# Performance work log

Measured on AMD Instinct MI355X. Metric: run time of the kernel, lower is better.

The kernel has to match this reference:

```python
import jax, jax.numpy as jnp
import numpy as np

WINDOW_SIZES = [4, 8, 12]
BN_EPS = 1e-5


def conv1x1(x, w, b):
    # x: [B,C,H,W], w: [O,C], b: [O]
    return jnp.einsum('bchw,oc->bohw', x, w) + b[None, :, None, None]


def bnorm(x, gamma, beta, mean, var):
    inv = gamma * jax.lax.rsqrt(var + BN_EPS)
    return (x - mean[None, :, None, None]) * inv[None, :, None, None] + beta[None, :, None, None]


def shift5(x):
    # ShiftConv2d1 depthwise fixed-weight conv == 4-direction zero-padded shift + identity
    b, c, H, W = x.shape
    g = c // 5
    p = jnp.pad(x, ((0, 0), (0, 0), (1, 1), (1, 1)))
    return jnp.concatenate([
        p[:, 0 * g:1 * g, 1:-1, 2:],    # kernel[1,2]: x[i, j+1]
        p[:, 1 * g:2 * g, 1:-1, :-2],   # kernel[1,0]: x[i, j-1]
        p[:, 2 * g:3 * g, 2:, 1:-1],    # kernel[2,1]: x[i+1, j]
        p[:, 3 * g:4 * g, :-2, 1:-1],   # kernel[0,1]: x[i-1, j]
        p[:, 4 * g:, 1:-1, 1:-1],       # kernel[1,1]: identity
    ], axis=1)


def lfe(x, w0, b0, w1, b1):
    y = jax.nn.relu(conv1x1(shift5(x), w0, b0))
    return conv1x1(shift5(y), w1, b1)


def win_part(x, ws):
    # [B,C,H,W] -> [B*nh*nw, ws*ws, C]
    b, c, H, W = x.shape
    x = x.reshape(b, c, H // ws, ws, W // ws, ws)
    return x.transpose(0, 2, 4, 3, 5, 1).reshape(b * (H // ws) * (W // ws), ws * ws, c)


def win_merge(y, ws, b, H, W):
    # [B*nh*nw, ws*ws, C] -> [B,C,H,W]
    c = y.shape[-1]
    y = y.reshape(b, H // ws, W // ws, ws, ws, c)
    return y.transpose(0, 5, 1, 3, 2, 4).reshape(b, c, H, W)


def gmsa_first(x, pi_w, pi_b, bn_g, bn_b, bn_m, bn_v, po_w, po_b):
    b, c, H, W = x.shape
    xp = bnorm(conv1x1(x, pi_w, pi_b), bn_g, bn_b, bn_m, bn_v)
    ch = 2 * c // 3
    ys, atns = [], []
    for i, ws in enumerate(WINDOW_SIZES):
        x_ = xp[:, i * ch:(i + 1) * ch]
        x_ = jnp.roll(x_, (-(ws // 2), -(ws // 2)), axis=(2, 3))
        qv = win_part(x_, ws)                      # [nw, ws*ws, 2*cc]
        cc = ch // 2
        q, v = qv[..., :cc], qv[..., cc:]
        atn = jax.nn.softmax(q @ q.transpose(0, 2, 1), axis=-1)
        y_ = win_merge(atn @ v, ws, b, H, W)
        y_ = jnp.roll(y_, (ws // 2, ws // 2), axis=(2, 3))
        ys.append(y_)
        atns.append(atn)
    return conv1x1(jnp.concatenate(ys, axis=1), po_w, po_b), atns


def gmsa_shared(x, atns, pi_w, pi_b, bn_g, bn_b, bn_m, bn_v, po_w, po_b):
    b, c, H, W = x.shape
    xp = bnorm(conv1x1(x, pi_w, pi_b), bn_g, bn_b, bn_m, bn_v)
    ch = c // 3
    ys = []
    for i, ws in enumerate(WINDOW_SIZES):
        x_ = jnp.roll(xp[:, i * ch:(i + 1) * ch], (-(ws // 2), -(ws // 2)), axis=(2, 3))
        v = win_part(x_, ws)
        y_ = win_merge(atns[i] @ v, ws, b, H, W)
        ys.append(jnp.roll(y_, (ws // 2, ws // 2), axis=(2, 3)))
    return conv1x1(jnp.concatenate(ys, axis=1), po_w, po_b)


def setup_inputs() -> dict:
    key = jax.random.key(0)
    ks = jax.random.split(key, 20)
    B, C, H, W = 4, 60, 384, 384
    E = 2 * C  # exp_ratio=2 hidden width
    s = 0.05

    def rn(k, shape):
        return jax.random.normal(k, shape, dtype=jnp.float32) * s

    return {
        'x': jax.random.normal(ks[0], (B, C, H, W), dtype=jnp.float32),
        # LFE 0
        'lfe0_w0': rn(ks[1], (E, C)), 'lfe0_b0': jnp.zeros((E,), jnp.float32),
        'lfe0_w1': rn(ks[2], (C, E)), 'lfe0_b1': jnp.zeros((C,), jnp.float32),
        # GMSA 0 (calc_attn=True): project_inp C->2C, BN(2C), project_out C->C
        'g0_pi_w': rn(ks[3], (2 * C, C)), 'g0_pi_b': jnp.zeros((2 * C,), jnp.float32),
        'g0_bn_g': jnp.ones((2 * C,), jnp.float32), 'g0_bn_b': jnp.zeros((2 * C,), jnp.float32),
        'g0_bn_m': jnp.zeros((2 * C,), jnp.float32), 'g0_bn_v': jnp.ones((2 * C,), jnp.float32),
        'g0_po_w': rn(ks[4], (C, C)), 'g0_po_b': jnp.zeros((C,), jnp.float32),
        # LFE 1
        'lfe1_w0': rn(ks[5], (E, C)), 'lfe1_b0': jnp.zeros((E,), jnp.float32),
        'lfe1_w1': rn(ks[6], (C, E)), 'lfe1_b1': jnp.zeros((C,), jnp.float32),
        # GMSA 1 (calc_attn=False): project_inp C->C, BN(C), project_out C->C
        'g1_pi_w': rn(ks[7], (C, C)), 'g1_pi_b': jnp.zeros((C,), jnp.float32),
        'g1_bn_g': jnp.ones((C,), jnp.float32), 'g1_bn_b': jnp.zeros((C,), jnp.float32),
        'g1_bn_m': jnp.zeros((C,), jnp.float32), 'g1_bn_v': jnp.ones((C,), jnp.float32),
        'g1_po_w': rn(ks[8], (C, C)), 'g1_po_b': jnp.zeros((C,), jnp.float32),
    }


def reference(x, lfe0_w0, lfe0_b0, lfe0_w1, lfe0_b1,
              g0_pi_w, g0_pi_b, g0_bn_g, g0_bn_b, g0_bn_m, g0_bn_v, g0_po_w, g0_po_b,
              lfe1_w0, lfe1_b0, lfe1_w1, lfe1_b1,
              g1_pi_w, g1_pi_b, g1_bn_g, g1_bn_b, g1_bn_m, g1_bn_v, g1_po_w, g1_po_b):
    # depth 0
    x = lfe(x, lfe0_w0, lfe0_b0, lfe0_w1, lfe0_b1) + x
    y, atns = gmsa_first(x, g0_pi_w, g0_pi_b, g0_bn_g, g0_bn_b, g0_bn_m, g0_bn_v, g0_po_w, g0_po_b)
    x = y + x
    # shared depth 1 (reuses attention maps)
    x = lfe(x, lfe1_w0, lfe1_b0, lfe1_w1, lfe1_b1) + x
    y = gmsa_shared(x, atns, g1_pi_w, g1_pi_b, g1_bn_g, g1_bn_b, g1_bn_m, g1_bn_v, g1_po_w, g1_po_b)
    return y + x
```

## Files before the change

kernel.cpp:

```cpp
#include <hip/hip_runtime.h>
#include <math.h>

constexpr int B_ = 4, C_ = 60, H_ = 384, W_ = 384;
constexpr int HW_ = H_ * W_;
constexpr int NC_ = B_ * C_ * HW_;
constexpr int NE_ = B_ * 120 * HW_;

typedef __attribute__((ext_vector_type(8))) short short8;
typedef __attribute__((ext_vector_type(4))) float f32x4;
typedef __attribute__((ext_vector_type(4))) unsigned short u16x4;

__device__ __forceinline__ unsigned short f2b(float f) {
    unsigned u = __builtin_bit_cast(unsigned, f);
    unsigned r = (u + 0x7fff + ((u >> 16) & 1)) >> 16;
    return (unsigned short)r;
}
__device__ __forceinline__ float b2f(unsigned short s) {
    return __builtin_bit_cast(float, (unsigned)s << 16);
}

__device__ __forceinline__ int xcd_swz(int bid, int nwg) {
    const int q = nwg >> 3, r = nwg & 7;
    const int xcd = bid & 7, off = bid >> 3;
    return (xcd < r ? xcd * (q + 1) : r * (q + 1) + (xcd - r) * q) + off;
}

struct PrepJobs {
    const float* src[8];
    unsigned short* dst[8];
    int cin[8];
    int cout[8];
};

__global__ __launch_bounds__(256) void prep_all(PrepJobs J)
{
    int bid = blockIdx.x;
    #pragma unroll 1
    for (int j = 0; j < 8; ++j) {
        const int KP = J.cin[j]  > 64 ? 128 : 64;
        const int MP = J.cout[j] > 64 ? 128 : 64;
        const int nb = MP * KP / 256;
        if (bid < nb) {
            const int i = bid * 256 + threadIdx.x;
            const int o = i / KP, c = i - o * KP;
            const float v = (o < J.cout[j] && c < J.cin[j]) ? J.src[j][o * J.cin[j] + c] : 0.f;
            J.dst[j][o * KP + (c ^ ((o & 7) << 3))] = f2b(v);
            return;
        }
        bid -= nb;
    }
}

struct ABJobs {
    const float* bias[8];
    const float* g[8];
    const float* bb[8];
    const float* m[8];
    const float* v[8];
    float* dst[8];
    int cout[8];
};

__global__ __launch_bounds__(256) void prep_ab(ABJobs J)
{
    const int j = blockIdx.x;
    const int n = J.cout[j];
    for (int o = threadIdx.x; o < n; o += 256) {
        float A = 1.f, Bv = J.bias[j][o];
        if (J.g[j]) {
            const float s = J.g[j][o] * rsqrtf(J.v[j][o] + 1e-5f);
            A  = s;
            Bv = (Bv - J.m[j][o]) * s + J.bb[j][o];
        }
        J.dst[j][o]     = A;
        J.dst[j][n + o] = Bv;
    }
}

template<int KP>
__device__ __forceinline__ int lds_off(int px, int cb) {
    return px * (KP * 2) + (cb ^ ((px & 7) << 4) ^ (((px >> 3) & 1) << 6));
}

template<int CIN, int COUT, int GSH, bool SRCB, bool RELU, bool RESID,
         bool RESIDB, bool OUTB>
__global__ __launch_bounds__(256, 4)
void conv_g(const void* __restrict__ in_, const unsigned short* __restrict__ wp,
            const float* __restrict__ AB,
            const void* __restrict__ resid_, void* __restrict__ out_)
{
    constexpr int KP  = CIN  > 64 ? 128 : 64;
    constexpr int MP  = COUT > 64 ? 128 : 64;
    constexpr int NNT = MP / 16;
    constexpr int KBL = KP / 32;
    __shared__ __align__(16) char xlds[128 * KP * 2];

    const int tid = threadIdx.x;
    const int n0  = blockIdx.x * 128;
    const int b   = n0 / HW_;
    const int p0  = n0 - b * HW_;
    const int hh  = p0 / W_;
    const int ww0 = p0 - hh * W_;

    for (int task = tid; task < (KP / 2) * 16; task += 256) {
        const int oct = (task >> 4) & 15;
        const int pr  = (task & 15) | ((task >> 8) << 4);
        const int c0  = pr * 2;
        const int s0  = oct * 8;

        if (c0 >= CIN) {
            #pragma unroll
            for (int i = 0; i < 8; ++i)
                *(unsigned*)(xlds + lds_off<KP>(s0 + i, c0 * 2)) = 0u;
            continue;
        }

        int dh = 0, dw = 0;
        if (GSH > 0) {
            const int grp = c0 / GSH;
            dh = (grp == 2) ? 1 : ((grp == 3) ? -1 : 0);
            dw = (grp == 0) ? 1 : ((grp == 1) ? -1 : 0);
        }
        const int h2 = hh + dh;
        const bool vh = (unsigned)h2 < (unsigned)H_;
        const long eoff = (long)(b * CIN + c0) * HW_ + h2 * W_ + ww0 + s0;

        unsigned short va[8], vb[8];
        if (vh) {
            if constexpr (SRCB) {
                const unsigned short* p = (const unsigned short*)in_;
                short8 A = *(const short8*)(p + eoff);
                short8 Bv = *(const short8*)(p + eoff + HW_);
                #pragma unroll
                for (int i = 0; i < 8; ++i) { va[i] = (unsigned short)A[i]; vb[i] = (unsigned short)Bv[i]; }
            } else {
                const float* p = (const float*)in_;
                f32x4 A0 = *(const f32x4*)(p + eoff);
                f32x4 A1 = *(const f32x4*)(p + eoff + 4);
                f32x4 B0 = *(const f32x4*)(p + eoff + HW_);
                f32x4 B1 = *(const f32x4*)(p + eoff + HW_ + 4);
                #pragma unroll
                for (int i = 0; i < 4; ++i) {
                    va[i] = f2b(A0[i]); va[i + 4] = f2b(A1[i]);
                    vb[i] = f2b(B0[i]); vb[i + 4] = f2b(B1[i]);
                }
            }
        } else {
            #pragma unroll
            for (int i = 0; i < 8; ++i) { va[i] = 0; vb[i] = 0; }
        }
        #pragma unroll
        for (int i = 0; i < 8; ++i) {
            const int px = s0 + i - dw;
            if ((unsigned)px < 128u) {
                const unsigned v = (unsigned)va[i] | ((unsigned)vb[i] << 16);
                *(unsigned*)(xlds + lds_off<KP>(px, c0 * 2)) = v;
            }
        }
        if (GSH > 0 && dw != 0) {
            const bool hndl = (dw == 1) ? (oct == 15) : (oct == 0);
            if (hndl) {
                const int px_e = (dw == 1) ? 127 : 0;
                const int w_abs = ww0 + px_e + dw;
                unsigned short ua = 0, ub = 0;
                if (vh && (unsigned)w_abs < (unsigned)W_) {
                    const long e2 = (long)(b * CIN + c0) * HW_ + h2 * W_ + w_abs;
                    if constexpr (SRCB) {
                        ua = ((const unsigned short*)in_)[e2];
                        ub = ((const unsigned short*)in_)[e2 + HW_];
                    } else {
                        ua = f2b(((const float*)in_)[e2]);
                        ub = f2b(((const float*)in_)[e2 + HW_]);
                    }
                }
                *(unsigned*)(xlds + lds_off<KP>(px_e, c0 * 2)) =
                    (unsigned)ua | ((unsigned)ub << 16);
            }
        }
    }
    __syncthreads();

    const int wv = tid >> 6, lo = tid & 15, hi = (tid & 63) >> 4;
    f32x4 acc[2][NNT];
    #pragma unroll
    for (int mt = 0; mt < 2; ++mt)
        #pragma unroll
        for (int nt = 0; nt < NNT; ++nt) acc[mt][nt] = f32x4{0.f, 0.f, 0.f, 0.f};

    #pragma unroll
    for (int kb = 0; kb < KBL; ++kb) {
        short8 a[2], bb[NNT];
        #pragma unroll
        for (int mt = 0; mt < 2; ++mt) {
            const int row = wv * 32 + mt * 16 + lo;
            a[mt] = *(const short8*)(xlds + lds_off<KP>(row, kb * 64 + hi * 16));
        }
        #pragma unroll
        for (int nt = 0; nt < NNT; ++nt) {
            const int row = nt * 16 + lo;
            bb[nt] = *(const short8*)((const char*)wp +
                      row * (KP * 2) + ((kb * 64 + hi * 16) ^ ((row & 7) << 4)));
        }
        #pragma unroll
        for (int mt = 0; mt < 2; ++mt)
            #pragma unroll
            for (int nt = 0; nt < NNT; ++nt)
                acc[mt][nt] = __builtin_amdgcn_mfma_f32_16x16x32_bf16(
                    a[mt], bb[nt], acc[mt][nt], 0, 0, 0);
    }

    #pragma unroll
    for (int mt = 0; mt < 2; ++mt) {
        const int px0 = p0 + wv * 32 + mt * 16 + hi * 4;
        #pragma unroll
        for (int nt = 0; nt < NNT; ++nt) {
            const int ch = nt * 16 + lo;
            if (ch < COUT) {
                const long oi = (long)(b * COUT + ch) * HW_ + px0;
                float v[4];
                f32x4 rf;
                u16x4 rb;
                if (RESID) {
                    if (RESIDB) rb = *(const u16x4*)((const unsigned short*)resid_ + oi);
                    else        rf = *(const f32x4*)((const float*)resid_ + oi);
                }
                #pragma unroll
                for (int r = 0; r < 4; ++r) {
                    float t = fmaf(acc[mt][nt][r], AB[ch], AB[COUT + ch]);
                    if (RELU) t = fmaxf(t, 0.f);
                    if (RESID) t += RESIDB ? b2f(rb[r]) : rf[r];
                    v[r] = t;
                }
                if (OUTB) {
                    u16x4 o4;
                    #pragma unroll
                    for (int r = 0; r < 4; ++r) o4[r] = f2b(v[r]);
                    *(u16x4*)((unsigned short*)out_ + oi) = o4;
                } else {
                    *(f32x4*)((float*)out_ + oi) = f32x4{v[0], v[1], v[2], v[3]};
                }
            }
        }
    }
}

template<int WS, int WPB>
__global__ __launch_bounds__(256)
void attn_m(const unsigned short* __restrict__ qsrc, int qC, int qbase,
            const unsigned short* __restrict__ vsrc, int vC, int vbase,
            unsigned short* __restrict__ out, int obase)
{
    constexpr int P     = WS * WS;
    constexpr int NMT   = P / 16;
    constexpr int S     = WS / 2;
    constexpr int WGX   = W_ / WS;
    constexpr int WGY   = H_ / WS;
    constexpr int NWIN  = WGY * WGX;
    constexpr int QP    = 40;
    constexpr int KP2   = ((P + 31) / 32) * 32;
    constexpr int VP    = KP2 + 8;
    constexpr int KB2   = KP2 / 32;
    constexpr int TILES = WPB * NMT;

    __shared__ __align__(16) unsigned short Qs[WPB * P * QP];
    __shared__ __align__(16) unsigned short VTs[WPB * 32 * VP];
    __shared__ __align__(16) unsigned short Ps[WPB * P * VP];
    __shared__ float rs[WPB * P];

    const int tid = threadIdx.x;
    const int blk = xcd_swz(blockIdx.x, gridDim.x);

    for (int i = tid; i < WPB * P * 6; i += 256) {
        const int row = i / 6, j = i - (i / 6) * 6;
        *(unsigned*)&Qs[row * QP + 20 + 2 * j] = 0u;
    }
    for (int i = tid; i < WPB * 12 * (KP2 / 2); i += 256) {
        const int rr = i / (KP2 / 2), j = i - rr * (KP2 / 2);
        const int win = rr / 12, ch = 20 + (rr - (rr / 12) * 12);
        *(unsigned*)&VTs[(win * 32 + ch) * VP + 2 * j] = 0u;
    }
    if constexpr (KP2 > P) {
        for (int i = tid; i < WPB * 20 * ((KP2 - P) / 2); i += 256) {
            const int rr = i / ((KP2 - P) / 2), j = i - rr * ((KP2 - P) / 2);
            const int win = rr / 20, ch = rr - (rr / 20) * 20;
            *(unsigned*)&VTs[(win * 32 + ch) * VP + P + 2 * j] = 0u;
        }
        for (int i = tid; i < WPB * P * ((KP2 - P) / 2); i += 256) {
            const int row = i / ((KP2 - P) / 2), j = i - row * ((KP2 - P) / 2);
            *(unsigned*)&Ps[row * VP + P + 2 * j] = 0u;
        }
    }
    for (int e = tid; e < WPB * P * 20; e += 256) {
        const int win = e / (P * 20);
        const int rem = e - win * (P * 20);
        const int ch  = rem / P;
        const int pos = rem - ch * P;
        const int gw  = blk * WPB + win;
        const int b   = gw / NWIN;
        const int rwin = gw - b * NWIN;
        const int wh = rwin / WGX, ww = rwin - (rwin / WGX) * WGX;
        const int pr = pos / WS,  pc = pos - (pos / WS) * WS;
        int hs = wh * WS + pr + S; if (hs >= H_) hs -= H_;
        int wd = ww * WS + pc + S; if (wd >= W_) wd -= W_;
        const long off = (long)hs * W_ + wd;
        Qs [(win * P  + pos) * QP + ch ] = qsrc[(long)(b * qC + qbase + ch) * HW_ + off];
        VTs[(win * 32 + ch ) * VP + pos] = vsrc[(long)(b * vC + vbase + ch) * HW_ + off];
    }
    __syncthreads();

    const int wv = tid >> 6, lo = tid & 15, hi = (tid & 63) >> 4;

    for (int t = wv; t < TILES; t += 4) {
        const int win = t / NMT, mt = t - (t / NMT) * NMT;
        const unsigned short* Qw = Qs + win * P * QP;
        unsigned short* Pw = Ps + win * P * VP;

        const short8 af = *(const short8*)(Qw + (mt * 16 + lo) * QP + hi * 8);
        f32x4 a1[NMT];
        #pragma unroll
        for (int nt = 0; nt < NMT; ++nt) a1[nt] = f32x4{0.f, 0.f, 0.f, 0.f};
        #pragma unroll
        for (int nt = 0; nt < NMT; ++nt) {
            const short8 bf = *(const short8*)(Qw + (nt * 16 + lo) * QP + hi * 8);
            a1[nt] = __builtin_amdgcn_mfma_f32_16x16x32_bf16(af, bf, a1[nt], 0, 0, 0);
        }
        float psum[4] = {0.f, 0.f, 0.f, 0.f};
        #pragma unroll
        for (int nt = 0; nt < NMT; ++nt) {
            #pragma unroll
            for (int r = 0; r < 4; ++r) {
                const float p = __expf(a1[nt][r]);
                psum[r] += p;
                Pw[(mt * 16 + hi * 4 + r) * VP + nt * 16 + lo] = f2b(p);
            }
        }
        #pragma unroll
        for (int r = 0; r < 4; ++r) {
            psum[r] += __shfl_xor(psum[r], 1);
            psum[r] += __shfl_xor(psum[r], 2);
            psum[r] += __shfl_xor(psum[r], 4);
            psum[r] += __shfl_xor(psum[r], 8);
        }
        if (lo == 0) {
            #pragma unroll
            for (int r = 0; r < 4; ++r)
                rs[win * P + mt * 16 + hi * 4 + r] = psum[r];
        }
    }
    __syncthreads();

    for (int t = wv; t < TILES; t += 4) {
        const int win = t / NMT, qt = t - (t / NMT) * NMT;
        const unsigned short* Vw = VTs + win * 32 * VP;
        const unsigned short* Pw = Ps + win * P * VP;

        f32x4 a2[2];
        a2[0] = f32x4{0.f, 0.f, 0.f, 0.f};
        a2[1] = f32x4{0.f, 0.f, 0.f, 0.f};
        #pragma unroll
        for (int kb = 0; kb < KB2; ++kb) {
            const short8 bf = *(const short8*)(Pw + (qt * 16 + lo) * VP + kb * 32 + hi * 8);
            #pragma unroll
            for (int m2 = 0; m2 < 2; ++m2) {
                const short8 af = *(const short8*)(Vw + (m2 * 16 + lo) * VP + kb * 32 + hi * 8);
                a2[m2] = __builtin_amdgcn_mfma_f32_16x16x32_bf16(af, bf, a2[m2], 0, 0, 0);
            }
        }
        const int gw = blk * WPB + win;
        const int b  = gw / NWIN;
        const int rwin = gw - b * NWIN;
        const int wh = rwin / WGX, ww = rwin - (rwin / WGX) * WGX;

        const int row = qt * 16 + lo;
        const float inv = 1.f / rs[win * P + row];
        const int pr = row / WS, pc = row - (row / WS) * WS;
        int hs = wh * WS + pr + S; if (hs >= H_) hs -= H_;
        int wd = ww * WS + pc + S; if (wd >= W_) wd -= W_;
        const long pbase = (long)(b * 60 + obase) * HW_ + (long)hs * W_ + wd;
        #pragma unroll
        for (int m2 = 0; m2 < 2; ++m2) {
            #pragma unroll
            for (int r = 0; r < 4; ++r) {
                const int ch = m2 * 16 + hi * 4 + r;
                if (ch < 20)
                    out[pbase + (long)ch * HW_] = f2b(a2[m2][r] * inv);
            }
        }
    }
}

extern "C" void kernel_launch(void* const* d_in, const int* in_sizes, int n_in,
                              void* d_out, int out_size, void* d_ws, size_t ws_size,
                              hipStream_t stream)
{
    const float* x     = (const float*)d_in[0];
    const float* l0w0  = (const float*)d_in[1];
    const float* l0b0  = (const float*)d_in[2];
    const float* l0w1  = (const float*)d_in[3];
    const float* l0b1  = (const float*)d_in[4];
    const float* g0piw = (const float*)d_in[5];
    const float* g0pib = (const float*)d_in[6];
    const float* g0bng = (const float*)d_in[7];
    const float* g0bnb = (const float*)d_in[8];
    const float* g0bnm = (const float*)d_in[9];
    const float* g0bnv = (const float*)d_in[10];
    const float* g0pow = (const float*)d_in[11];
    const float* g0pob = (const float*)d_in[12];
    const float* l1w0  = (const float*)d_in[13];
    const float* l1b0  = (const float*)d_in[14];
    const float* l1w1  = (const float*)d_in[15];
    const float* l1b1  = (const float*)d_in[16];
    const float* g1piw = (const float*)d_in[17];
    const float* g1pib = (const float*)d_in[18];
    const float* g1bng = (const float*)d_in[19];
    const float* g1bnb = (const float*)d_in[20];
    const float* g1bnm = (const float*)d_in[21];
    const float* g1bnv = (const float*)d_in[22];
    const float* g1pow = (const float*)d_in[23];
    const float* g1pob = (const float*)d_in[24];

    unsigned short* HID = (unsigned short*)d_ws;
    unsigned short* XPB = HID + NE_;
    unsigned short* XP1 = XPB + NE_;
    unsigned short* YS1 = XP1 + NC_;
    unsigned short* CCB = YS1 + NC_;
    unsigned short* WP  = CCB + NC_;
    float*          ABF = (float*)(WP + 53248);
    float* OUTF  = (float*)d_out;
    unsigned short* YS0 = (unsigned short*)d_out;

    unsigned short* W1  = WP;
    unsigned short* W2  = WP + 8192;
    unsigned short* W3  = WP + 16384;
    unsigned short* W5  = WP + 24576;
    unsigned short* W6  = WP + 28672;
    unsigned short* W7  = WP + 36864;
    unsigned short* W8  = WP + 45056;
    unsigned short* W10 = WP + 49152;

    float* AB1  = ABF;
    float* AB2  = ABF + 240;
    float* AB3  = ABF + 360;
    float* AB5  = ABF + 600;
    float* AB6  = ABF + 720;
    float* AB7  = ABF + 960;
    float* AB8  = ABF + 1080;
    float* AB10 = ABF + 1200;

    PrepJobs J;
    J.src[0]=l0w0;  J.dst[0]=W1;  J.cin[0]=60;  J.cout[0]=120;
    J.src[1]=l0w1;  J.dst[1]=W2;  J.cin[1]=120; J.cout[1]=60;
    J.src[2]=g0piw; J.dst[2]=W3;  J.cin[2]=60;  J.cout[2]=120;
    J.src[3]=g0pow; J.dst[3]=W5;  J.cin[3]=60;  J.cout[3]=60;
    J.src[4]=l1w0;  J.dst[4]=W6;  J.cin[4]=60;  J.cout[4]=120;
    J.src[5]=l1w1;  J.dst[5]=W7;  J.cin[5]=120; J.cout[5]=60;
    J.src[6]=g1piw; J.dst[6]=W8;  J.cin[6]=60;  J.cout[6]=60;
    J.src[7]=g1pow; J.dst[7]=W10; J.cin[7]=60;  J.cout[7]=60;
    prep_all<<<208, 256, 0, stream>>>(J);

    ABJobs A;
    for (int j = 0; j < 8; ++j) { A.g[j]=nullptr; A.bb[j]=nullptr; A.m[j]=nullptr; A.v[j]=nullptr; }
    A.bias[0]=l0b0;  A.dst[0]=AB1;  A.cout[0]=120;
    A.bias[1]=l0b1;  A.dst[1]=AB2;  A.cout[1]=60;
    A.bias[2]=g0pib; A.dst[2]=AB3;  A.cout[2]=120; A.g[2]=g0bng; A.bb[2]=g0bnb; A.m[2]=g0bnm; A.v[2]=g0bnv;
    A.bias[3]=g0pob; A.dst[3]=AB5;  A.cout[3]=60;
    A.bias[4]=l1b0;  A.dst[4]=AB6;  A.cout[4]=120;
    A.bias[5]=l1b1;  A.dst[5]=AB7;  A.cout[5]=60;
    A.bias[6]=g1pib; A.dst[6]=AB8;  A.cout[6]=60;  A.g[6]=g1bng; A.bb[6]=g1bnb; A.m[6]=g1bnm; A.v[6]=g1bnv;
    A.bias[7]=g1pob; A.dst[7]=AB10; A.cout[7]=60;
    prep_ab<<<8, 256, 0, stream>>>(A);

    dim3 blk(256);
    dim3 gconv(B_ * HW_ / 128);

    conv_g<60,120,12,false,true,false,false,true><<<gconv,blk,0,stream>>>(
        x, W1, AB1, nullptr, HID);
    conv_g<120,60,24,true,false,true,false,true><<<gconv,blk,0,stream>>>(
        HID, W2, AB2, x, CCB);
    conv_g<60,120,0,true,false,false,false,true><<<gconv,blk,0,stream>>>(
        CCB, W3, AB3, nullptr, XPB);
    attn_m<4,4><<<dim3(9216),blk,0,stream>>>(XPB,120,0,   XPB,120,20,  YS0, 0);
    attn_m<8,1><<<dim3(9216),blk,0,stream>>>(XPB,120,40,  XPB,120,60,  YS0,20);
    attn_m<12,1><<<dim3(4096),blk,0,stream>>>(XPB,120,80, XPB,120,100, YS0,40);
    conv_g<60,60,0,true,false,true,true,true><<<gconv,blk,0,stream>>>(
        YS0, W5, AB5, CCB, CCB);
    conv_g<60,120,12,true,true,false,false,true><<<gconv,blk,0,stream>>>(
        CCB, W6, AB6, nullptr, HID);
    conv_g<120,60,24,true,false,true,true,true><<<gconv,blk,0,stream>>>(
        HID, W7, AB7, CCB, CCB);
    conv_g<60,60,0,true,false,false,false,true><<<gconv,blk,0,stream>>>(
        CCB, W8, AB8, nullptr, XP1);
    attn_m<4,4><<<dim3(9216),blk,0,stream>>>(XPB,120,0,  XP1,60,0,  YS1, 0);
    attn_m<8,1><<<dim3(9216),blk,0,stream>>>(XPB,120,40, XP1,60,20, YS1,20);
    attn_m<12,1><<<dim3(4096),blk,0,stream>>>(XPB,120,80,XP1,60,40, YS1,40);
    conv_g<60,60,0,true,false,true,true,false><<<gconv,blk,0,stream>>>(
        YS1, W10, AB10, CCB, OUTF);
}
```

Before: 981.9 us.

## Add specialized 120->60 shift-conv kernel with split-K double-buffered LDS staging

New measurement: 989.0 us. No clear change (+0.7%).

```diff
diff --git a/kernel.cpp b/kernel.cpp
--- a/kernel.cpp
+++ b/kernel.cpp
@@ -239,6 +239,179 @@
                 } else {
                     *(f32x4*)((float*)out_ + oi) = f32x4{v[0], v[1], v[2], v[3]};
                 }
+            }
+        }
+    }
+}
+
+template<bool RESIDB, bool OUTB>
+__global__ __launch_bounds__(256, 4)
+void conv_g2(const unsigned short* __restrict__ in_,
+             const unsigned short* __restrict__ wp,
+             const float* __restrict__ AB,
+             const void* __restrict__ resid_, void* __restrict__ out_)
+{
+    constexpr int COUT = 60;
+    constexpr int NNT  = 4;
+    __shared__ __align__(16) char xlds[2][128 * 128];
+
+    const int tid = threadIdx.x;
+    const int n0  = blockIdx.x * 128;
+    const int b   = n0 / HW_;
+    const int p0  = n0 - b * HW_;
+    const int hh  = p0 / W_;
+    const int ww0 = p0 - hh * W_;
+
+    auto h_load = [&](int task, int h, short8& A, short8& Bv, unsigned& edge) {
+        const int oct = (task >> 5) & 15;
+        const int pr  = task & 31;
+        const int c0g = h * 64 + pr * 2;
+        A = short8{0,0,0,0,0,0,0,0}; Bv = A; edge = 0;
+        if (c0g >= 120) return;
+        const int grp = c0g / 24;
+        const int dh = (grp == 2) ? 1 : ((grp == 3) ? -1 : 0);
+        const int dw = (grp == 0) ? 1 : ((grp == 1) ? -1 : 0);
+        const int h2 = hh + dh;
+        const bool vh = (unsigned)h2 < (unsigned)H_;
+        const int s0 = oct * 8;
+        const long eoff = (long)(b * 120 + c0g) * HW_ + h2 * W_ + ww0 + s0;
+        if (vh) {
+            A  = *(const short8*)(in_ + eoff);
+            Bv = *(const short8*)(in_ + eoff + HW_);
+        }
+        if (dw != 0) {
+            const bool hndl = (dw == 1) ? (oct == 15) : (oct == 0);
+            if (hndl) {
+                const int px_e = (dw == 1) ? 127 : 0;
+                const int w_abs = ww0 + px_e + dw;
+                if (vh && (unsigned)w_abs < (unsigned)W_) {
+                    const long e2 = (long)(b * 120 + c0g) * HW_ + h2 * W_ + w_abs;
+                    edge = (unsigned)in_[e2] | ((unsigned)in_[e2 + HW_] << 16);
+                }
+            }
+        }
+    };
+    auto h_write = [&](int task, int h, short8 A, short8 Bv, unsigned edge) {
+        const int oct = (task >> 5) & 15;
+        const int pr  = task & 31;
+        const int c0g = h * 64 + pr * 2;
+        const int cb  = pr * 4;
+        const int s0  = oct * 8;
+        int dw = 0;
+        if (c0g < 120) {
+            const int grp = c0g / 24;
+            dw = (grp == 0) ? 1 : ((grp == 1) ? -1 : 0);
+        }
+        #pragma unroll
+        for (int j = 0; j < 8; ++j) {
+            const int px = s0 + j - dw;
+            if ((unsigned)px < 128u) {
+                const unsigned v = (unsigned)(unsigned short)A[j] |
+                                   ((unsigned)(unsigned short)Bv[j] << 16);
+                *(unsigned*)(xlds[h] + lds_off<64>(px, cb)) = v;
+            }
+        }
+        if (dw != 0) {
+            const bool hndl = (dw == 1) ? (oct == 15) : (oct == 0);
+            if (hndl) {
+                const int px_e = (dw == 1) ? 127 : 0;
+                *(unsigned*)(xlds[h] + lds_off<64>(px_e, cb)) = edge;
+            }
+        }
+    };
+
+    {
+        short8 A0, B0, A1, B1; unsigned e0, e1;
+        h_load(tid,       0, A0, B0, e0);
+        h_load(tid + 256, 0, A1, B1, e1);
+        h_write(tid,       0, A0, B0, e0);
+        h_write(tid + 256, 0, A1, B1, e1);
+    }
+    __syncthreads();
+
+    short8 pA0, pB0, pA1, pB1; unsigned pe0, pe1;
+    h_load(tid,       1, pA0, pB0, pe0);
+    h_load(tid + 256, 1, pA1, pB1, pe1);
+
+    const int wv = tid >> 6, lo = tid & 15, hi = (tid & 63) >> 4;
+    f32x4 acc[2][NNT];
+    #pragma unroll
+    for (int mt = 0; mt < 2; ++mt)
+        #pragma unroll
+        for (int nt = 0; nt < NNT; ++nt) acc[mt][nt] = f32x4{0.f, 0.f, 0.f, 0.f};
+
+    #pragma unroll
+    for (int kb = 0; kb < 2; ++kb) {
+        short8 a[2], bb[NNT];
+        #pragma unroll
+        for (int mt = 0; mt < 2; ++mt) {
+            const int row = wv * 32 + mt * 16 + lo;
+            a[mt] = *(const short8*)(xlds[0] + lds_off<64>(row, kb * 64 + hi * 16));
+        }
+        #pragma unroll
+        for (int nt = 0; nt < NNT; ++nt) {
+            const int row = nt * 16 + lo;
+            bb[nt] = *(const short8*)((const char*)wp +
+                      row * 256 + ((kb * 64 + hi * 16) ^ ((row & 7) << 4)));
+        }
+        #pragma unroll
+        for (int mt = 0; mt < 2; ++mt)
+            #pragma unroll
+            for (int nt = 0; nt < NNT; ++nt)
+                acc[mt][nt] = __builtin_amdgcn_mfma_f32_16x16x32_bf16(
+                    a[mt], bb[nt], acc[mt][nt], 0, 0, 0);
+    }
+
+    h_write(tid,       1, pA0, pB0, pe0);
+    h_write(tid + 256, 1, pA1, pB1, pe1);
+    __syncthreads();
+
+    #pragma unroll
+    for (int kb = 0; kb < 2; ++kb) {
+        const int kbg = 2 + kb;
+        short8 a[2], bb[NNT];
+        #pragma unroll
+        for (int mt = 0; mt < 2; ++mt) {
+            const int row = wv * 32 + mt * 16 + lo;
+            a[mt] = *(const short8*)(xlds[1] + lds_off<64>(row, kb * 64 + hi * 16));
+        }
+        #pragma unroll
+        for (int nt = 0; nt < NNT; ++nt) {
+            const int row = nt * 16 + lo;
+            bb[nt] = *(const short8*)((const char*)wp +
+                      row * 256 + ((kbg * 64 + hi * 16) ^ ((row & 7) << 4)));
+        }
+        #pragma unroll
+        for (int mt = 0; mt < 2; ++mt)
+            #pragma unroll
+            for (int nt = 0; nt < NNT; ++nt)
+                acc[mt][nt] = __builtin_amdgcn_mfma_f32_16x16x32_bf16(
+                    a[mt], bb[nt], acc[mt][nt], 0, 0, 0);
+    }
+
+    #pragma unroll
+    for (int mt = 0; mt < 2; ++mt) {
+        const int px0 = p0 + wv * 32 + mt * 16 + hi * 4;
+        #pragma unroll
+        for (int nt = 0; nt < NNT; ++nt) {
+            const int ch = nt * 16 + lo;
+            if (ch < COUT) {
+                const long oi = (long)(b * COUT + ch) * HW_ + px0;
+                float v[4];
+                f32x4 rf;
+                u16x4 rb;
+                if (RESIDB) rb = *(const u16x4*)((const unsigned short*)resid_ + oi);
+                else        rf = *(const f32x4*)((const float*)resid_ + oi);
+                #pragma unroll
+                for (int r = 0; r < 4; ++r) {
+                    float t = fmaf(acc[mt][nt][r], AB[ch], AB[COUT + ch]);
+                    t += RESIDB ? b2f(rb[r]) : rf[r];
+                    v[r] = t;
+                }
+                u16x4 o4;
+                #pragma unroll
+                for (int r = 0; r < 4; ++r) o4[r] = f2b(v[r]);
+                *(u16x4*)((unsigned short*)out_ + oi) = o4;
             }
         }
     }
@@ -475,8 +648,7 @@
 
     conv_g<60,120,12,false,true,false,false,true><<<gconv,blk,0,stream>>>(
         x, W1, AB1, nullptr, HID);
-    conv_g<120,60,24,true,false,true,false,true><<<gconv,blk,0,stream>>>(
-        HID, W2, AB2, x, CCB);
+    conv_g2<false,true><<<gconv,blk,0,stream>>>(HID, W2, AB2, x, CCB);
     conv_g<60,120,0,true,false,false,false,true><<<gconv,blk,0,stream>>>(
         CCB, W3, AB3, nullptr, XPB);
     attn_m<4,4><<<dim3(9216),blk,0,stream>>>(XPB,120,0,   XPB,120,20,  YS0, 0);
@@ -486,8 +658,7 @@
         YS0, W5, AB5, CCB, CCB);
     conv_g<60,120,12,true,true,false,false,true><<<gconv,blk,0,stream>>>(
         CCB, W6, AB6, nullptr, HID);
-    conv_g<120,60,24,true,false,true,true,true><<<gconv,blk,0,stream>>>(
-        HID, W7, AB7, CCB, CCB);
+    conv_g2<true,true><<<gconv,blk,0,stream>>>(HID, W7, AB7, CCB, CCB);
     conv_g<60,60,0,true,false,false,false,true><<<gconv,blk,0,stream>>>(
         CCB, W8, AB8, nullptr, XP1);
     attn_m<4,4><<<dim3(9216),blk,0,stream>>>(XPB,120,0,  XP1,60,0,  YS1, 0);
```
